# Kernel optimization log

Hardware: AMD Instinct MI355X
Metric: run time of the kernel (lower is better)

The kernel has to match this reference:

```python
import jax, jax.numpy as jnp
import numpy as np

BITS = 8
EPS = 1e-08


def _scalar_quantize_maxabs(x, scale, bits, eps):
    # clamp(round(x / scale), -qmax, qmax) with a fixed (precomputed) scalar scale
    qmax = float(2 ** (bits - 1) - 1)
    s = jnp.maximum(scale, eps)
    return jnp.clip(jnp.round(x / s), -qmax, qmax)


def setup_inputs() -> dict:
    key = jax.random.key(0)
    k1, k2, k3 = jax.random.split(key, 3)
    B, S, D_in, D_out = 4, 2048, 2048, 2048
    hidden_states = jax.random.normal(k1, (B, S, D_in), dtype=jnp.float32)
    # weight_quantized holds low-bit integer values stored as float (as produced by the quantizer)
    qmax = float(2 ** (BITS - 1) - 1)
    weight_quantized = jnp.round(
        jnp.clip(jax.random.normal(k2, (D_in, D_out), dtype=jnp.float32) * (qmax / 3.0), -qmax, qmax)
    )
    x_scale = jnp.asarray(0.05, dtype=jnp.float32)
    bias = jax.random.normal(k3, (D_out,), dtype=jnp.float32)
    return {
        "hidden_states": hidden_states,
        "weight_quantized": weight_quantized,
        "x_scale": x_scale,
        "bias": bias,
    }


def reference(hidden_states, weight_quantized, x_scale, bias) -> jnp.ndarray:
    original_shape = hidden_states.shape[:-1]
    input_dim = hidden_states.shape[-1]
    x_flat = hidden_states.reshape(-1, input_dim)  # [B*S, D_in]
    x_q = _scalar_quantize_maxabs(x_flat, x_scale.reshape(()), BITS, EPS)
    out = x_q.astype(weight_quantized.dtype) @ weight_quantized  # [B*S, D_out]
    out = out + bias.astype(out.dtype)[None, :]
    return out.astype(hidden_states.dtype).reshape(*original_shape, weight_quantized.shape[1])
```

## Files before the change

### kernel.cpp

```cpp
#include <hip/hip_runtime.h>
#include <cstdint>
#include <cstddef>

#define MDIM 8192
#define NDIM 2048
#define KDIM 2048

constexpr int BM = 128, BN = 128, BK = 64;

typedef int v4i __attribute__((ext_vector_type(4)));

__device__ __forceinline__ void async_ld16(const void* g, void* l) {
    __builtin_amdgcn_global_load_lds(
        (const __attribute__((address_space(1))) int*)g,
        (__attribute__((address_space(3))) int*)l,
        16, 0, 0);
}

__device__ __forceinline__ int q8(float x, float s) {
    float q = fminf(fmaxf(rintf(x / s), -127.f), 127.f);
    return ((int)q) & 0xff;
}

__global__ void quant_x_kernel(const float* __restrict__ x, uint32_t* __restrict__ xq,
                               const float* __restrict__ scale_p) {
    int i = blockIdx.x * blockDim.x + threadIdx.x;
    float s = fmaxf(scale_p[0], 1e-8f);
    float4 v = reinterpret_cast<const float4*>(x)[i];
    uint32_t p = (uint32_t)q8(v.x, s)
               | ((uint32_t)q8(v.y, s) << 8)
               | ((uint32_t)q8(v.z, s) << 16)
               | ((uint32_t)q8(v.w, s) << 24);
    xq[i] = p;
}

__global__ void quant_wt_kernel(const float* __restrict__ w, int8_t* __restrict__ wt) {
    __shared__ int8_t t[64][65];
    const int k0 = blockIdx.y * 64;
    const int n0 = blockIdx.x * 64;
    const int tid = threadIdx.x;
    const int rr = tid >> 4;
    const int c4 = (tid & 15) * 4;
    for (int p = 0; p < 4; ++p) {
        int r = rr + p * 16;
        float4 v = *(const float4*)&w[(size_t)(k0 + r) * NDIM + n0 + c4];
        t[c4 + 0][r] = (int8_t)rintf(v.x);
        t[c4 + 1][r] = (int8_t)rintf(v.y);
        t[c4 + 2][r] = (int8_t)rintf(v.z);
        t[c4 + 3][r] = (int8_t)rintf(v.w);
    }
    __syncthreads();
    for (int p = 0; p < 4; ++p) {
        int c = rr + p * 16;
        uint32_t o = (uint32_t)(uint8_t)t[c][c4 + 0]
                   | ((uint32_t)(uint8_t)t[c][c4 + 1] << 8)
                   | ((uint32_t)(uint8_t)t[c][c4 + 2] << 16)
                   | ((uint32_t)(uint8_t)t[c][c4 + 3] << 24);
        *(uint32_t*)&wt[(size_t)(n0 + c) * KDIM + k0 + c4] = o;
    }
}

__global__ __launch_bounds__(256, 2)
void gemm_i8_kernel(const int8_t* __restrict__ A,
                    const int8_t* __restrict__ Bt,
                    const float* __restrict__ bias,
                    float* __restrict__ C) {
    __shared__ alignas(16) int8_t lA[BM * BK];
    __shared__ alignas(16) int8_t lB[BN * BK];

    const int tid  = threadIdx.x;
    const int lane = tid & 63;
    const int wave = tid >> 6;
    const int wm   = wave & 1;
    const int wn   = wave >> 1;
    const int m0   = blockIdx.y * BM;
    const int n0   = blockIdx.x * BN;

    const int r0 = wave * 32 + (lane >> 2);
    const int r1 = r0 + 16;
    const int kk = (lane & 3) * 16;
    const int8_t* gA0 = A  + (size_t)(m0 + r0) * KDIM + kk;
    const int8_t* gA1 = A  + (size_t)(m0 + r1) * KDIM + kk;
    const int8_t* gB0 = Bt + (size_t)(n0 + r0) * KDIM + kk;
    const int8_t* gB1 = Bt + (size_t)(n0 + r1) * KDIM + kk;
    int8_t* ldsA0 = &lA[wave * 2048];
    int8_t* ldsA1 = &lA[wave * 2048 + 1024];
    int8_t* ldsB0 = &lB[wave * 2048];
    int8_t* ldsB1 = &lB[wave * 2048 + 1024];

    const int quad = lane >> 4;
    const int lr   = lane & 15;
    const int aoff = (wm * 64 + lr) * BK + quad * 16;
    const int boff = (wn * 64 + lr) * BK + quad * 16;

    v4i acc[4][4];
    for (int i = 0; i < 4; ++i)
        for (int j = 0; j < 4; ++j)
            acc[i][j] = (v4i){0, 0, 0, 0};

    for (int k0 = 0; k0 < KDIM; k0 += BK) {
        __syncthreads();
        async_ld16(gA0, ldsA0);
        async_ld16(gA1, ldsA1);
        async_ld16(gB0, ldsB0);
        async_ld16(gB1, ldsB1);
        gA0 += BK; gA1 += BK; gB0 += BK; gB1 += BK;
        __syncthreads();

        v4i af[4], bf[4];
        for (int i = 0; i < 4; ++i)
            af[i] = *(const v4i*)&lA[aoff + i * 16 * BK];
        for (int j = 0; j < 4; ++j)
            bf[j] = *(const v4i*)&lB[boff + j * 16 * BK];
        for (int i = 0; i < 4; ++i)
            for (int j = 0; j < 4; ++j)
                acc[i][j] = __builtin_amdgcn_mfma_i32_16x16x64_i8(af[i], bf[j], acc[i][j], 0, 0, 0);
    }

    const int crow = m0 + wm * 64 + quad * 4;
    const int ccol = n0 + wn * 64 + lr;
    float bj[4];
    for (int j = 0; j < 4; ++j) bj[j] = bias[ccol + j * 16];
    for (int i = 0; i < 4; ++i) {
        for (int j = 0; j < 4; ++j) {
            for (int r = 0; r < 4; ++r) {
                int row = crow + i * 16 + r;
                int col = ccol + j * 16;
                C[(size_t)row * NDIM + col] = (float)acc[i][j][r] + bj[j];
            }
        }
    }
}

extern "C" void kernel_launch(void* const* d_in, const int* in_sizes, int n_in,
                              void* d_out, int out_size, void* d_ws, size_t ws_size,
                              hipStream_t stream) {
    const float* x    = (const float*)d_in[0];
    const float* w    = (const float*)d_in[1];
    const float* xs   = (const float*)d_in[2];
    const float* bias = (const float*)d_in[3];
    float* out = (float*)d_out;

    int8_t* xq = (int8_t*)d_ws;
    int8_t* wt = xq + (size_t)MDIM * KDIM;

    quant_x_kernel<<<(MDIM * (KDIM / 4)) / 256, 256, 0, stream>>>(x, (uint32_t*)xq, xs);
    quant_wt_kernel<<<dim3(NDIM / 64, KDIM / 64), 256, 0, stream>>>(w, wt);
    gemm_i8_kernel<<<dim3(NDIM / BN, MDIM / BM), 256, 0, stream>>>(xq, wt, bias, out);
}
```

Measured before the change: 173.3 us.

## Double GEMM K-tile with XOR-swizzled LDS and vectorize activation quantization

The GEMM K-tile doubles to 128 and LDS gets an XOR chunk swizzle to avoid bank conflicts, which halves the number of barrier pairs per K sweep. Launch bounds move to 4 blocks per SM. Activation quantization now multiplies by a precomputed reciprocal and writes 16 bytes per thread. The reciprocal can round differently from a true divide at ties, and the larger LDS footprint and register cap may limit occupancy.

```diff
diff --git a/kernel.cpp b/kernel.cpp
--- a/kernel.cpp
+++ b/kernel.cpp
@@ -6,7 +6,7 @@
 #define NDIM 2048
 #define KDIM 2048
 
-constexpr int BM = 128, BN = 128, BK = 64;
+constexpr int BM = 128, BN = 128, BK = 128;
 
 typedef int v4i __attribute__((ext_vector_type(4)));
 
@@ -17,21 +17,22 @@
         16, 0, 0);
 }
 
-__device__ __forceinline__ int q8(float x, float s) {
-    float q = fminf(fmaxf(rintf(x / s), -127.f), 127.f);
-    return ((int)q) & 0xff;
+__device__ __forceinline__ uint32_t q8(float x, float inv) {
+    float q = fminf(fmaxf(rintf(x * inv), -127.f), 127.f);
+    return (uint32_t)((int)q) & 0xffu;
 }
 
-__global__ void quant_x_kernel(const float* __restrict__ x, uint32_t* __restrict__ xq,
+__global__ void quant_x_kernel(const float4* __restrict__ x, uint4* __restrict__ xq,
                                const float* __restrict__ scale_p) {
-    int i = blockIdx.x * blockDim.x + threadIdx.x;
-    float s = fmaxf(scale_p[0], 1e-8f);
-    float4 v = reinterpret_cast<const float4*>(x)[i];
-    uint32_t p = (uint32_t)q8(v.x, s)
-               | ((uint32_t)q8(v.y, s) << 8)
-               | ((uint32_t)q8(v.z, s) << 16)
-               | ((uint32_t)q8(v.w, s) << 24);
-    xq[i] = p;
+    int t = blockIdx.x * blockDim.x + threadIdx.x;
+    float inv = 1.0f / fmaxf(scale_p[0], 1e-8f);
+    uint32_t w[4];
+#pragma unroll
+    for (int j = 0; j < 4; ++j) {
+        float4 v = x[t * 4 + j];
+        w[j] = q8(v.x, inv) | (q8(v.y, inv) << 8) | (q8(v.z, inv) << 16) | (q8(v.w, inv) << 24);
+    }
+    xq[t] = make_uint4(w[0], w[1], w[2], w[3]);
 }
 
 __global__ void quant_wt_kernel(const float* __restrict__ w, int8_t* __restrict__ wt) {
@@ -60,7 +61,7 @@
     }
 }
 
-__global__ __launch_bounds__(256, 2)
+__global__ __launch_bounds__(256, 4)
 void gemm_i8_kernel(const int8_t* __restrict__ A,
                     const int8_t* __restrict__ Bt,
                     const float* __restrict__ bias,
@@ -76,60 +77,66 @@
     const int m0   = blockIdx.y * BM;
     const int n0   = blockIdx.x * BN;
 
-    const int r0 = wave * 32 + (lane >> 2);
-    const int r1 = r0 + 16;
-    const int kk = (lane & 3) * 16;
-    const int8_t* gA0 = A  + (size_t)(m0 + r0) * KDIM + kk;
-    const int8_t* gA1 = A  + (size_t)(m0 + r1) * KDIM + kk;
-    const int8_t* gB0 = Bt + (size_t)(n0 + r0) * KDIM + kk;
-    const int8_t* gB1 = Bt + (size_t)(n0 + r1) * KDIM + kk;
-    int8_t* ldsA0 = &lA[wave * 2048];
-    int8_t* ldsA1 = &lA[wave * 2048 + 1024];
-    int8_t* ldsB0 = &lB[wave * 2048];
-    int8_t* ldsB1 = &lB[wave * 2048 + 1024];
+    const int srow = lane >> 3;
+    const int schk = (lane & 7) ^ srow;
+    const int8_t* gA = A  + (size_t)(m0 + wave * 32 + srow) * KDIM + schk * 16;
+    const int8_t* gB = Bt + (size_t)(n0 + wave * 32 + srow) * KDIM + schk * 16;
+    int8_t* lAw = &lA[wave * 4096];
+    int8_t* lBw = &lB[wave * 4096];
 
     const int quad = lane >> 4;
     const int lr   = lane & 15;
-    const int aoff = (wm * 64 + lr) * BK + quad * 16;
-    const int boff = (wn * 64 + lr) * BK + quad * 16;
+    const int sw   = lr & 7;
+    const int arow = (wm * 64 + lr) * BK;
+    const int brow = (wn * 64 + lr) * BK;
 
     v4i acc[4][4];
+#pragma unroll
     for (int i = 0; i < 4; ++i)
+#pragma unroll
         for (int j = 0; j < 4; ++j)
             acc[i][j] = (v4i){0, 0, 0, 0};
 
     for (int k0 = 0; k0 < KDIM; k0 += BK) {
         __syncthreads();
-        async_ld16(gA0, ldsA0);
-        async_ld16(gA1, ldsA1);
-        async_ld16(gB0, ldsB0);
-        async_ld16(gB1, ldsB1);
-        gA0 += BK; gA1 += BK; gB0 += BK; gB1 += BK;
+#pragma unroll
+        for (int i = 0; i < 4; ++i) {
+            async_ld16(gA + (size_t)i * 8 * KDIM, lAw + i * 1024);
+            async_ld16(gB + (size_t)i * 8 * KDIM, lBw + i * 1024);
+        }
+        gA += BK; gB += BK;
         __syncthreads();
 
-        v4i af[4], bf[4];
-        for (int i = 0; i < 4; ++i)
-            af[i] = *(const v4i*)&lA[aoff + i * 16 * BK];
-        for (int j = 0; j < 4; ++j)
-            bf[j] = *(const v4i*)&lB[boff + j * 16 * BK];
-        for (int i = 0; i < 4; ++i)
+#pragma unroll
+        for (int s = 0; s < 2; ++s) {
+            const int cs = ((4 * s + quad) ^ sw) * 16;
+            v4i af[4], bf[4];
+#pragma unroll
+            for (int i = 0; i < 4; ++i)
+                af[i] = *(const v4i*)&lA[arow + i * 16 * BK + cs];
+#pragma unroll
             for (int j = 0; j < 4; ++j)
-                acc[i][j] = __builtin_amdgcn_mfma_i32_16x16x64_i8(af[i], bf[j], acc[i][j], 0, 0, 0);
+                bf[j] = *(const v4i*)&lB[brow + j * 16 * BK + cs];
+#pragma unroll
+            for (int i = 0; i < 4; ++i)
+#pragma unroll
+                for (int j = 0; j < 4; ++j)
+                    acc[i][j] = __builtin_amdgcn_mfma_i32_16x16x64_i8(af[i], bf[j], acc[i][j], 0, 0, 0);
+        }
     }
 
     const int crow = m0 + wm * 64 + quad * 4;
     const int ccol = n0 + wn * 64 + lr;
     float bj[4];
+#pragma unroll
     for (int j = 0; j < 4; ++j) bj[j] = bias[ccol + j * 16];
-    for (int i = 0; i < 4; ++i) {
-        for (int j = 0; j < 4; ++j) {
-            for (int r = 0; r < 4; ++r) {
-                int row = crow + i * 16 + r;
-                int col = ccol + j * 16;
-                C[(size_t)row * NDIM + col] = (float)acc[i][j][r] + bj[j];
-            }
-        }
-    }
+#pragma unroll
+    for (int i = 0; i < 4; ++i)
+#pragma unroll
+        for (int j = 0; j < 4; ++j)
+#pragma unroll
+            for (int r = 0; r < 4; ++r)
+                C[(size_t)(crow + i * 16 + r) * NDIM + (ccol + j * 16)] = (float)acc[i][j][r] + bj[j];
 }
 
 extern "C" void kernel_launch(void* const* d_in, const int* in_sizes, int n_in,
@@ -144,7 +151,8 @@
     int8_t* xq = (int8_t*)d_ws;
     int8_t* wt = xq + (size_t)MDIM * KDIM;
 
-    quant_x_kernel<<<(MDIM * (KDIM / 4)) / 256, 256, 0, stream>>>(x, (uint32_t*)xq, xs);
+    quant_x_kernel<<<((size_t)MDIM * KDIM / 16) / 256, 256, 0, stream>>>(
+        (const float4*)x, (uint4*)xq, xs);
     quant_wt_kernel<<<dim3(NDIM / 64, KDIM / 64), 256, 0, stream>>>(w, wt);
     gemm_i8_kernel<<<dim3(NDIM / BN, MDIM / BM), 256, 0, stream>>>(xq, wt, bias, out);
 }
```

Result: faster. 168.7 us (-2.6%).
